# Kernel tuning notes

Hardware: AMD Instinct MI355X
Metric: run time of the kernel (lower is better)

The kernel has to match this reference:

```python
import jax, jax.numpy as jnp
import numpy as np

DIMS = [128, 118, 109, 100, 92]  # dims[i+1] = max(int(dims[i]/1.081), 6)
NUM_SHELLS = 3
TARGET_COORD = 1.081
NUM_BASINS = 8
BATCH = 12288


def _pdist(a, b):
    # Euclidean pairwise distances [Na, Nb]
    a2 = jnp.sum(a * a, axis=-1)
    b2 = jnp.sum(b * b, axis=-1)
    d2 = a2[:, None] + b2[None, :] - 2.0 * (a @ b.T)
    return jnp.sqrt(jnp.clip(d2, 0.0, None))


def setup_inputs() -> dict:
    key = jax.random.key(0)
    ks = jax.random.split(key, 32)
    inp = {"x": jax.random.normal(ks[0], (BATCH, DIMS[0]), jnp.float32)}
    i = 1
    for s in range(4):
        din, dout = DIMS[s], DIMS[s + 1]
        sc = 1.0 / np.sqrt(din)
        inp[f"cw{s}"] = jax.random.uniform(ks[i], (dout, din), jnp.float32, -sc, sc); i += 1
        inp[f"cb{s}"] = jax.random.uniform(ks[i], (dout,), jnp.float32, -sc, sc); i += 1
        sc0 = 1.0 / np.sqrt(DIMS[0])
        inp[f"sw{s}"] = jax.random.uniform(ks[i], (dout, DIMS[0]), jnp.float32, -sc0, sc0); i += 1
        inp[f"sb{s}"] = jax.random.uniform(ks[i], (dout,), jnp.float32, -sc0, sc0); i += 1
    D = DIMS[-1]
    inp["shell_bnd"] = jnp.linspace(0.5, 2.0, NUM_SHELLS + 1, dtype=jnp.float32)
    scs = 1.0 / np.sqrt(NUM_SHELLS)
    inp["se_w"] = jax.random.uniform(ks[i], (D, NUM_SHELLS), jnp.float32, -scs, scs); i += 1
    inp["se_b"] = jax.random.uniform(ks[i], (D,), jnp.float32, -scs, scs); i += 1
    inp["basin_c"] = jax.random.normal(ks[i], (NUM_BASINS, D), jnp.float32) * 0.1; i += 1
    inp["basin_d"] = jnp.linspace(-6.48, -7.68, NUM_BASINS, dtype=jnp.float32)
    inp["basin_w"] = jnp.ones((NUM_BASINS,), jnp.float32) * 0.5
    return inp


def _forward(x, cws, cbs, sws, sbs, shell_bnd, se_w, se_b, basin_c, basin_d, basin_w):
    # CompressionTransform: Linear -> GELU (+ 0.1 * skip from input)
    cur = x
    for w, b, w2, b2 in zip(cws, cbs, sws, sbs):
        cur = jax.nn.gelu(cur @ w.T + b, approximate=False) + 0.1 * (x @ w2.T + b2)
    compressed = cur  # [B, 92]

    # EnergyLandscape: softmax basin mixture
    bdists = _pdist(compressed, basin_c)             # [B, num_basins]
    widths = jax.nn.softplus(basin_w)                # [num_basins]
    basin_probs = jax.nn.softmax(-bdists / widths, axis=-1)
    energy = jnp.sum(basin_probs * basin_d, axis=-1)  # [B]

    # CoordinationAnalysis: pairwise-distance shell histogram
    B = compressed.shape[0]
    dself = _pdist(compressed, compressed)           # [B, B]
    offdiag = ~jnp.eye(B, dtype=bool)
    bnd = jax.nn.softplus(shell_bnd)
    occ = jnp.stack(
        [jnp.sum(jnp.where(offdiag & (dself >= bnd[i]) & (dself < bnd[i + 1]), 1.0, 0.0), axis=-1)
         for i in range(NUM_SHELLS)],
        axis=-1,
    )  # [B, num_shells]
    occ = occ / (TARGET_COORD * (B - 1) + 1e-08)
    feats = compressed + occ @ se_w.T + se_b          # features with coordination info
    return feats, energy, basin_probs, occ


def reference(x, cw0, cb0, sw0, sb0, cw1, cb1, sw1, sb1, cw2, cb2, sw2, sb2,
              cw3, cb3, sw3, sb3, shell_bnd, se_w, se_b, basin_c, basin_d, basin_w):
    cws = [cw0, cw1, cw2, cw3]
    cbs = [cb0, cb1, cb2, cb3]
    sws = [sw0, sw1, sw2, sw3]
    sbs = [sb0, sb1, sb2, sb3]
    return _forward(x, cws, cbs, sws, sbs, shell_bnd, se_w, se_b, basin_c, basin_d, basin_w)
```

## Files before the change

kernel.cpp:

```cpp
#include <hip/hip_runtime.h>
#include <hip/hip_bf16.h>

typedef __attribute__((ext_vector_type(8))) short bf16x8;
typedef __attribute__((ext_vector_type(4))) float f32x4;
typedef unsigned short u16;

#define BATCH 12288

__device__ __forceinline__ u16 f2bf(float f){
  __hip_bfloat16 h = __float2bfloat16(f);
  return *reinterpret_cast<u16*>(&h);
}
__device__ __forceinline__ float bf2f(u16 u){
  __hip_bfloat16 h; *reinterpret_cast<u16*>(&h) = u;
  return __bfloat162float(h);
}
__device__ __forceinline__ f32x4 mfma16(bf16x8 a, bf16x8 b, f32x4 c){
  return __builtin_amdgcn_mfma_f32_16x16x32_bf16(a, b, c, 0, 0, 0);
}
__device__ __forceinline__ float softplusf(float v){ return log1pf(expf(v)); }

__global__ __launch_bounds__(256) void k_wconv8(
    const float* __restrict__ s0, const float* __restrict__ s1,
    const float* __restrict__ s2, const float* __restrict__ s3,
    const float* __restrict__ s4, const float* __restrict__ s5,
    const float* __restrict__ s6, const float* __restrict__ s7,
    u16* __restrict__ dst)
{
  int blk = blockIdx.x;
  int slab = blk >> 6;
  const float* src; int rows, cols;
  switch (slab){
    case 0: src = s0; rows = 118; cols = 128; break;
    case 1: src = s1; rows = 118; cols = 128; break;
    case 2: src = s2; rows = 109; cols = 118; break;
    case 3: src = s3; rows = 109; cols = 128; break;
    case 4: src = s4; rows = 100; cols = 109; break;
    case 5: src = s5; rows = 100; cols = 128; break;
    case 6: src = s6; rows =  92; cols = 100; break;
    default: src = s7; rows =  92; cols = 128; break;
  }
  int idx = (blk & 63) * 256 + threadIdx.x;
  int r = idx >> 7, c = idx & 127;
  float v = (r < rows && c < cols) ? src[r * cols + c] : 0.f;
  dst[slab * 16384 + idx] = f2bf(v);
}

__global__ __launch_bounds__(256) void k_mlp(const float* __restrict__ x,
    const u16* __restrict__ slabs,
    const float* __restrict__ cb0, const float* __restrict__ cb1,
    const float* __restrict__ cb2, const float* __restrict__ cb3,
    const float* __restrict__ sb0, const float* __restrict__ sb1,
    const float* __restrict__ sb2, const float* __restrict__ sb3,
    float* __restrict__ comp)
{
  const int LSTR = 136;
  __shared__ u16 xbf[32 * 136];
  __shared__ u16 act[2][32 * 136];
  int tid = threadIdx.x;
  int lane = tid & 63, w = tid >> 6;
  int fr = lane & 15, fg = lane >> 4;
  int r0 = blockIdx.x * 32;

  #pragma unroll
  for (int i = 0; i < 4; i++){
    int slot = tid + i * 256;
    int row = slot >> 5, c4 = slot & 31;
    float4 v = *reinterpret_cast<const float4*>(&x[(r0 + row) * 128 + c4 * 4]);
    ushort4 pk;
    pk.x = f2bf(v.x); pk.y = f2bf(v.y); pk.z = f2bf(v.z); pk.w = f2bf(v.w);
    *reinterpret_cast<ushort4*>(&xbf[row * LSTR + c4 * 4]) = pk;
  }
  __syncthreads();

  bf16x8 xa[2][4];
  #pragma unroll
  for (int mf = 0; mf < 2; mf++)
    #pragma unroll
    for (int kc = 0; kc < 4; kc++)
      xa[mf][kc] = *reinterpret_cast<const bf16x8*>(&xbf[(16*mf + fr) * LSTR + kc*32 + fg*8]);

  const float* cbs[4] = {cb0, cb1, cb2, cb3};
  const float* sbs[4] = {sb0, sb1, sb2, sb3};
  const int douts[4] = {118, 109, 100, 92};

  #pragma unroll
  for (int s = 0; s < 4; s++){
    const u16* aIn  = (s == 0) ? xbf : &act[(s + 1) & 1][0];
    u16*       aOut = &act[s & 1][0];
    const u16* cwS = slabs + (2*s)     * 16384;
    const u16* swS = slabs + (2*s + 1) * 16384;
    const float* cb = cbs[s];
    const float* sb = sbs[s];
    int dout = douts[s];

    bf16x8 af[2][4];
    #pragma unroll
    for (int mf = 0; mf < 2; mf++)
      #pragma unroll
      for (int kc = 0; kc < 4; kc++)
        af[mf][kc] = *reinterpret_cast<const bf16x8*>(&aIn[(16*mf + fr) * LSTR + kc*32 + fg*8]);

    f32x4 ac1[2][2], ac2[2][2];
    #pragma unroll
    for (int mf = 0; mf < 2; mf++)
      #pragma unroll
      for (int nf = 0; nf < 2; nf++){
        ac1[mf][nf] = (f32x4){0.f,0.f,0.f,0.f};
        ac2[mf][nf] = (f32x4){0.f,0.f,0.f,0.f};
      }

    #pragma unroll
    for (int nf = 0; nf < 2; nf++){
      int o = 32*w + 16*nf + fr;
      #pragma unroll
      for (int kc = 0; kc < 4; kc++){
        bf16x8 b1 = *reinterpret_cast<const bf16x8*>(&cwS[o * 128 + kc*32 + fg*8]);
        bf16x8 b2 = *reinterpret_cast<const bf16x8*>(&swS[o * 128 + kc*32 + fg*8]);
        ac1[0][nf] = mfma16(af[0][kc], b1, ac1[0][nf]);
        ac1[1][nf] = mfma16(af[1][kc], b1, ac1[1][nf]);
        ac2[0][nf] = mfma16(xa[0][kc], b2, ac2[0][nf]);
        ac2[1][nf] = mfma16(xa[1][kc], b2, ac2[1][nf]);
      }
    }

    #pragma unroll
    for (int nf = 0; nf < 2; nf++){
      int col = 32*w + 16*nf + fr;
      float cbv = (col < dout) ? cb[col] : 0.f;
      float sbv = (col < dout) ? sb[col] : 0.f;
      #pragma unroll
      for (int mf = 0; mf < 2; mf++){
        #pragma unroll
        for (int r = 0; r < 4; r++){
          float t1 = ac1[mf][nf][r] + cbv;
          float g = 0.5f * t1 * (1.f + erff(t1 * 0.70710678118654752f));
          float v = g + 0.1f * (ac2[mf][nf][r] + sbv);
          int row = 16*mf + fg*4 + r;
          if (s < 3){
            aOut[row * LSTR + col] = (col < dout) ? f2bf(v) : (u16)0;
          } else {
            if (col < 92) comp[(r0 + row) * 92 + col] = v;
          }
        }
      }
    }
    __syncthreads();
  }
}

__global__ __launch_bounds__(256) void k_rowfin(const float* __restrict__ comp,
    u16* __restrict__ Cbf, float* __restrict__ nrm,
    const float* __restrict__ basin_c, const float* __restrict__ basin_d,
    const float* __restrict__ basin_w,
    float* __restrict__ energy_out, float* __restrict__ probs_out)
{
  int tid = threadIdx.x; int lane = tid & 63; int w = tid >> 6;
  int row = blockIdx.x * 4 + w;

  float c0 = comp[row * 92 + lane];
  int d2i = 64 + lane;
  float c1 = (d2i < 92) ? comp[row * 92 + d2i] : 0.f;

  u16 b0 = f2bf(c0);
  u16 b1 = (d2i < 92) ? f2bf(c1) : (u16)0;
  Cbf[row * 96 + lane] = b0;
  if (lane < 32) Cbf[row * 96 + 64 + lane] = b1;

  float f0 = bf2f(b0), f1 = bf2f(b1);
  float ns = f0*f0 + f1*f1;
  #pragma unroll
  for (int m = 1; m < 64; m <<= 1) ns += __shfl_xor(ns, m);
  if (lane == 0) nrm[row] = ns;

  float bd[8];
  #pragma unroll
  for (int b = 0; b < 8; b++){
    float e0 = c0 - basin_c[b * 92 + lane];
    float p = e0 * e0;
    if (d2i < 92){ float e1 = c1 - basin_c[b * 92 + d2i]; p += e1 * e1; }
    #pragma unroll
    for (int m = 1; m < 64; m <<= 1) p += __shfl_xor(p, m);
    bd[b] = sqrtf(p);
  }
  float z[8]; float mx = -1e30f;
  #pragma unroll
  for (int b = 0; b < 8; b++){
    float wd = softplusf(basin_w[b]);
    z[b] = -bd[b] / wd;
    mx = fmaxf(mx, z[b]);
  }
  float p8[8]; float ssum = 0.f;
  #pragma unroll
  for (int b = 0; b < 8; b++){ p8[b] = expf(z[b] - mx); ssum += p8[b]; }
  float inv = 1.f / ssum; float en = 0.f;
  #pragma unroll
  for (int b = 0; b < 8; b++){ p8[b] *= inv; en += p8[b] * basin_d[b]; }

  if (lane == 0) energy_out[row] = en;
  if (lane < 8){
    float v = (lane & 4) ? ((lane & 2) ? ((lane & 1) ? p8[7] : p8[6])
                                       : ((lane & 1) ? p8[5] : p8[4]))
                         : ((lane & 2) ? ((lane & 1) ? p8[3] : p8[2])
                                       : ((lane & 1) ? p8[1] : p8[0]));
    probs_out[row * 8 + lane] = v;
  }
}

__global__ __launch_bounds__(256, 4) void k_pdist(const u16* __restrict__ Cbf,
    const float* __restrict__ nrm, const float* __restrict__ shell_bnd,
    unsigned* __restrict__ cnt)
{
  __shared__ u16 Bs[2][64 * 104];
  __shared__ float Ns[2][64];
  int tid = threadIdx.x; int lane = tid & 63; int w = tid >> 6;
  int fr = lane & 15, fg = lane >> 4;
  int blk = blockIdx.x;
  int ib = blk % 96, jc = blk / 96;
  int i0 = ib * 128, j0 = jc * 384;

  float q0 = softplusf(shell_bnd[0]); q0 *= q0;
  float q1 = softplusf(shell_bnd[1]); q1 *= q1;
  float q2 = softplusf(shell_bnd[2]); q2 *= q2;
  float q3 = softplusf(shell_bnd[3]); q3 *= q3;

  int wrow0 = i0 + 32 * w;
  bf16x8 A[2][3];
  #pragma unroll
  for (int mf = 0; mf < 2; mf++)
    #pragma unroll
    for (int kc = 0; kc < 3; kc++)
      A[mf][kc] = *reinterpret_cast<const bf16x8*>(&Cbf[(wrow0 + 16*mf + fr) * 96 + kc*32 + fg*8]);

  float na[2][4];
  #pragma unroll
  for (int mf = 0; mf < 2; mf++)
    #pragma unroll
    for (int r = 0; r < 4; r++)
      na[mf][r] = nrm[wrow0 + 16*mf + fg*4 + r];

  unsigned c[2][4][4];
  #pragma unroll
  for (int mf = 0; mf < 2; mf++)
    #pragma unroll
    for (int r = 0; r < 4; r++)
      #pragma unroll
      for (int t = 0; t < 4; t++) c[mf][r][t] = 0u;

  auto stage = [&](int st, int p){
    int jr0 = j0 + st * 64;
    #pragma unroll
    for (int t = 0; t < 3; t++){
      int ch = tid + t * 256;
      int rr = ch / 12, sl = ch - rr * 12;
      *reinterpret_cast<bf16x8*>(&Bs[p][rr * 104 + sl * 8]) =
        *reinterpret_cast<const bf16x8*>(&Cbf[(jr0 + rr) * 96 + sl * 8]);
    }
    if (tid < 64) Ns[p][tid] = nrm[jr0 + tid];
  };

  auto hist = [&](f32x4 h0, f32x4 h1, float nb){
    float d2[2][4];
    #pragma unroll
    for (int r = 0; r < 4; r++){
      d2[0][r] = fmaf(-2.f, h0[r], na[0][r] + nb);
      d2[1][r] = fmaf(-2.f, h1[r], na[1][r] + nb);
    }
    float mn = d2[0][0];
    #pragma unroll
    for (int r = 1; r < 4; r++) mn = fminf(mn, d2[0][r]);
    #pragma unroll
    for (int r = 0; r < 4; r++) mn = fminf(mn, d2[1][r]);
    if (__any(mn < q3)){
      #pragma unroll
      for (int mf = 0; mf < 2; mf++)
        #pragma unroll
        for (int r = 0; r < 4; r++){
          float v = d2[mf][r];
          c[mf][r][0] += (v >= q0);
          c[mf][r][1] += (v >= q1);
          c[mf][r][2] += (v >= q2);
          c[mf][r][3] += (v >= q3);
        }
    }
  };

  stage(0, 0);
  __syncthreads();

  f32x4 gp0, gp1; float nbp = 0.f;
  gp0 = (f32x4){0.f,0.f,0.f,0.f}; gp1 = (f32x4){0.f,0.f,0.f,0.f};

  for (int s = 0; s < 6; s++){
    int p = s & 1;
    if (s < 5) stage(s + 1, p ^ 1);

    #pragma unroll
    for (int nt = 0; nt < 4; nt++){
      bf16x8 B0 = *reinterpret_cast<const bf16x8*>(&Bs[p][(nt*16 + fr) * 104 + 0*32 + fg*8]);
      bf16x8 B1 = *reinterpret_cast<const bf16x8*>(&Bs[p][(nt*16 + fr) * 104 + 1*32 + fg*8]);
      bf16x8 B2 = *reinterpret_cast<const bf16x8*>(&Bs[p][(nt*16 + fr) * 104 + 2*32 + fg*8]);
      float nb = Ns[p][nt*16 + fr];

      f32x4 g0 = (f32x4){0.f,0.f,0.f,0.f};
      f32x4 g1 = (f32x4){0.f,0.f,0.f,0.f};
      g0 = mfma16(A[0][0], B0, g0); g0 = mfma16(A[0][1], B1, g0); g0 = mfma16(A[0][2], B2, g0);
      g1 = mfma16(A[1][0], B0, g1); g1 = mfma16(A[1][1], B1, g1); g1 = mfma16(A[1][2], B2, g1);

      if (nt > 0 || s > 0) hist(gp0, gp1, nbp);

      gp0 = g0; gp1 = g1; nbp = nb;
    }
    __syncthreads();
  }
  hist(gp0, gp1, nbp);

  #pragma unroll
  for (int mf = 0; mf < 2; mf++)
    #pragma unroll
    for (int r = 0; r < 4; r++)
      #pragma unroll
      for (int t = 0; t < 4; t++){
        int v = (int)c[mf][r][t];
        v += __shfl_xor(v, 1); v += __shfl_xor(v, 2);
        v += __shfl_xor(v, 4); v += __shfl_xor(v, 8);
        c[mf][r][t] = (unsigned)v;
      }
  if (fr == 0){
    #pragma unroll
    for (int mf = 0; mf < 2; mf++)
      #pragma unroll
      for (int r = 0; r < 4; r++){
        int row = wrow0 + 16*mf + fg*4 + r;
        #pragma unroll
        for (int s = 0; s < 3; s++){
          unsigned o = c[mf][r][s] - c[mf][r][s + 1];
          if (o) atomicAdd(&cnt[row * 3 + s], o);
        }
      }
  }
}

__global__ __launch_bounds__(256) void k_feats(const float* __restrict__ comp,
    const unsigned* __restrict__ cnt, const float* __restrict__ se_w,
    const float* __restrict__ se_b, float* __restrict__ feats_out,
    float* __restrict__ occ_out)
{
  int tid = threadIdx.x; int lane = tid & 63; int w = tid >> 6;
  int row = blockIdx.x * 4 + w;
  const float denom = 1.081f * 12287.0f + 1e-8f;

  float o0 = (float)cnt[row * 3 + 0] / denom;
  float o1 = (float)cnt[row * 3 + 1] / denom;
  float o2 = (float)cnt[row * 3 + 2] / denom;

  {
    int d = lane;
    float v = comp[row * 92 + d]
            + o0 * se_w[d * 3 + 0] + o1 * se_w[d * 3 + 1] + o2 * se_w[d * 3 + 2]
            + se_b[d];
    feats_out[row * 92 + d] = v;
  }
  int d2 = lane + 64;
  if (d2 < 92){
    float v = comp[row * 92 + d2]
            + o0 * se_w[d2 * 3 + 0] + o1 * se_w[d2 * 3 + 1] + o2 * se_w[d2 * 3 + 2]
            + se_b[d2];
    feats_out[row * 92 + d2] = v;
  }
  if (lane < 3){
    float ov = (lane == 0) ? o0 : ((lane == 1) ? o1 : o2);
    occ_out[row * 3 + lane] = ov;
  }
}

extern "C" void kernel_launch(void* const* d_in, const int* in_sizes, int n_in,
                              void* d_out, int out_size, void* d_ws, size_t ws_size,
                              hipStream_t stream) {
  (void)in_sizes; (void)n_in; (void)out_size; (void)ws_size;

  const float* x = (const float*)d_in[0];
  const float* cw[4] = {(const float*)d_in[1], (const float*)d_in[5], (const float*)d_in[9],  (const float*)d_in[13]};
  const float* cb[4] = {(const float*)d_in[2], (const float*)d_in[6], (const float*)d_in[10], (const float*)d_in[14]};
  const float* sw[4] = {(const float*)d_in[3], (const float*)d_in[7], (const float*)d_in[11], (const float*)d_in[15]};
  const float* sb[4] = {(const float*)d_in[4], (const float*)d_in[8], (const float*)d_in[12], (const float*)d_in[16]};
  const float* shell_bnd = (const float*)d_in[17];
  const float* se_w = (const float*)d_in[18];
  const float* se_b = (const float*)d_in[19];
  const float* basin_c = (const float*)d_in[20];
  const float* basin_d = (const float*)d_in[21];
  const float* basin_w = (const float*)d_in[22];

  char* ws = (char*)d_ws;
  float*    comp  = (float*)(ws);
  u16*      Cbf   = (u16*)  (ws + 4521984);
  float*    nrm   = (float*)(ws + 6881280);
  unsigned* cnt   = (unsigned*)(ws + 6930432);
  u16*      slabs = (u16*)  (ws + 7077888);

  float* out = (float*)d_out;
  float* feats_out  = out;
  float* energy_out = out + 1130496;
  float* probs_out  = out + 1142784;
  float* occ_out    = out + 1241088;

  hipMemsetAsync(cnt, 0, 147456, stream);

  k_wconv8<<<512, 256, 0, stream>>>(cw[0], sw[0], cw[1], sw[1], cw[2], sw[2], cw[3], sw[3],
                                    slabs);

  k_mlp<<<384, 256, 0, stream>>>(x, slabs,
      cb[0], cb[1], cb[2], cb[3], sb[0], sb[1], sb[2], sb[3], comp);

  k_rowfin<<<3072, 256, 0, stream>>>(comp, Cbf, nrm, basin_c, basin_d, basin_w,
                                     energy_out, probs_out);

  k_pdist<<<3072, 256, 0, stream>>>(Cbf, nrm, shell_bnd, cnt);

  k_feats<<<3072, 256, 0, stream>>>(comp, cnt, se_w, se_b, feats_out, occ_out);
}
```

Baseline: 143.8 us.

## Fold norms into MFMA accumulator and register-stage pdist tile loads

Row norms are stored as -0.5*|x|^2 so the pairwise-distance test becomes a comparison of (hr + hc + dot) against -0.5*q^2. The norm sum is used as the MFMA initial accumulator, which removes the per-element fma. The global-to-LDS staging is split into a register load issued before the compute and an LDS write after it, so the global load latency overlaps the MFMAs. The __any early-out and the one-tile software pipeline of the histogram are dropped, and comparisons are now done unconditionally. This removes a branch at the cost of always doing the compares, and the negated scaling could shift rounding at the shell boundaries.

```diff
diff --git a/kernel.cpp b/kernel.cpp
--- a/kernel.cpp
+++ b/kernel.cpp
@@ -150,7 +150,7 @@
 }
 
 __global__ __launch_bounds__(256) void k_rowfin(const float* __restrict__ comp,
-    u16* __restrict__ Cbf, float* __restrict__ nrm,
+    u16* __restrict__ Cbf, float* __restrict__ nrm2,
     const float* __restrict__ basin_c, const float* __restrict__ basin_d,
     const float* __restrict__ basin_w,
     float* __restrict__ energy_out, float* __restrict__ probs_out)
@@ -171,7 +171,7 @@
   float ns = f0*f0 + f1*f1;
   #pragma unroll
   for (int m = 1; m < 64; m <<= 1) ns += __shfl_xor(ns, m);
-  if (lane == 0) nrm[row] = ns;
+  if (lane == 0) nrm2[row] = -0.5f * ns;
 
   float bd[8];
   #pragma unroll
@@ -208,7 +208,7 @@
 }
 
 __global__ __launch_bounds__(256, 4) void k_pdist(const u16* __restrict__ Cbf,
-    const float* __restrict__ nrm, const float* __restrict__ shell_bnd,
+    const float* __restrict__ nrm2, const float* __restrict__ shell_bnd,
     unsigned* __restrict__ cnt)
 {
   __shared__ u16 Bs[2][64 * 104];
@@ -219,10 +219,10 @@
   int ib = blk % 96, jc = blk / 96;
   int i0 = ib * 128, j0 = jc * 384;
 
-  float q0 = softplusf(shell_bnd[0]); q0 *= q0;
-  float q1 = softplusf(shell_bnd[1]); q1 *= q1;
-  float q2 = softplusf(shell_bnd[2]); q2 *= q2;
-  float q3 = softplusf(shell_bnd[3]); q3 *= q3;
+  float q0 = softplusf(shell_bnd[0]); float mq0 = -0.5f * q0 * q0;
+  float q1 = softplusf(shell_bnd[1]); float mq1 = -0.5f * q1 * q1;
+  float q2 = softplusf(shell_bnd[2]); float mq2 = -0.5f * q2 * q2;
+  float q3 = softplusf(shell_bnd[3]); float mq3 = -0.5f * q3 * q3;
 
   int wrow0 = i0 + 32 * w;
   bf16x8 A[2][3];
@@ -232,12 +232,12 @@
     for (int kc = 0; kc < 3; kc++)
       A[mf][kc] = *reinterpret_cast<const bf16x8*>(&Cbf[(wrow0 + 16*mf + fr) * 96 + kc*32 + fg*8]);
 
-  float na[2][4];
+  float hr[2][4];
   #pragma unroll
   for (int mf = 0; mf < 2; mf++)
     #pragma unroll
     for (int r = 0; r < 4; r++)
-      na[mf][r] = nrm[wrow0 + 16*mf + fg*4 + r];
+      hr[mf][r] = nrm2[wrow0 + 16*mf + fg*4 + r];
 
   unsigned c[2][4][4];
   #pragma unroll
@@ -247,73 +247,69 @@
       #pragma unroll
       for (int t = 0; t < 4; t++) c[mf][r][t] = 0u;
 
-  auto stage = [&](int st, int p){
+  int ofsL[3], ofsR[3], ofsS[3];
+  #pragma unroll
+  for (int t = 0; t < 3; t++){
+    int ch = tid + t * 256;
+    int rr = ch / 12, sl = ch - rr * 12;
+    ofsR[t] = rr; ofsS[t] = sl * 8;
+    ofsL[t] = rr * 104 + sl * 8;
+  }
+
+  bf16x8 rv[3]; float nsv = 0.f;
+  auto stage_load = [&](int st){
     int jr0 = j0 + st * 64;
     #pragma unroll
-    for (int t = 0; t < 3; t++){
-      int ch = tid + t * 256;
-      int rr = ch / 12, sl = ch - rr * 12;
-      *reinterpret_cast<bf16x8*>(&Bs[p][rr * 104 + sl * 8]) =
-        *reinterpret_cast<const bf16x8*>(&Cbf[(jr0 + rr) * 96 + sl * 8]);
-    }
-    if (tid < 64) Ns[p][tid] = nrm[jr0 + tid];
+    for (int t = 0; t < 3; t++)
+      rv[t] = *reinterpret_cast<const bf16x8*>(&Cbf[(jr0 + ofsR[t]) * 96 + ofsS[t]]);
+    if (tid < 64) nsv = nrm2[jr0 + tid];
   };
-
-  auto hist = [&](f32x4 h0, f32x4 h1, float nb){
-    float d2[2][4];
-    #pragma unroll
-    for (int r = 0; r < 4; r++){
-      d2[0][r] = fmaf(-2.f, h0[r], na[0][r] + nb);
-      d2[1][r] = fmaf(-2.f, h1[r], na[1][r] + nb);
-    }
-    float mn = d2[0][0];
-    #pragma unroll
-    for (int r = 1; r < 4; r++) mn = fminf(mn, d2[0][r]);
-    #pragma unroll
-    for (int r = 0; r < 4; r++) mn = fminf(mn, d2[1][r]);
-    if (__any(mn < q3)){
-      #pragma unroll
-      for (int mf = 0; mf < 2; mf++)
-        #pragma unroll
-        for (int r = 0; r < 4; r++){
-          float v = d2[mf][r];
-          c[mf][r][0] += (v >= q0);
-          c[mf][r][1] += (v >= q1);
-          c[mf][r][2] += (v >= q2);
-          c[mf][r][3] += (v >= q3);
-        }
-    }
+  auto stage_write = [&](int p){
+    #pragma unroll
+    for (int t = 0; t < 3; t++)
+      *reinterpret_cast<bf16x8*>(&Bs[p][ofsL[t]]) = rv[t];
+    if (tid < 64) Ns[p][tid] = nsv;
   };
 
-  stage(0, 0);
+  stage_load(0); stage_write(0);
   __syncthreads();
-
-  f32x4 gp0, gp1; float nbp = 0.f;
-  gp0 = (f32x4){0.f,0.f,0.f,0.f}; gp1 = (f32x4){0.f,0.f,0.f,0.f};
 
   for (int s = 0; s < 6; s++){
     int p = s & 1;
-    if (s < 5) stage(s + 1, p ^ 1);
+    if (s < 5) stage_load(s + 1);
 
     #pragma unroll
     for (int nt = 0; nt < 4; nt++){
       bf16x8 B0 = *reinterpret_cast<const bf16x8*>(&Bs[p][(nt*16 + fr) * 104 + 0*32 + fg*8]);
       bf16x8 B1 = *reinterpret_cast<const bf16x8*>(&Bs[p][(nt*16 + fr) * 104 + 1*32 + fg*8]);
       bf16x8 B2 = *reinterpret_cast<const bf16x8*>(&Bs[p][(nt*16 + fr) * 104 + 2*32 + fg*8]);
-      float nb = Ns[p][nt*16 + fr];
-
-      f32x4 g0 = (f32x4){0.f,0.f,0.f,0.f};
-      f32x4 g1 = (f32x4){0.f,0.f,0.f,0.f};
+      float hc = Ns[p][nt*16 + fr];
+
+      f32x4 g0, g1;
+      #pragma unroll
+      for (int r = 0; r < 4; r++){ g0[r] = hr[0][r] + hc; g1[r] = hr[1][r] + hc; }
       g0 = mfma16(A[0][0], B0, g0); g0 = mfma16(A[0][1], B1, g0); g0 = mfma16(A[0][2], B2, g0);
       g1 = mfma16(A[1][0], B0, g1); g1 = mfma16(A[1][1], B1, g1); g1 = mfma16(A[1][2], B2, g1);
 
-      if (nt > 0 || s > 0) hist(gp0, gp1, nbp);
-
-      gp0 = g0; gp1 = g1; nbp = nb;
+      #pragma unroll
+      for (int r = 0; r < 4; r++){
+        float v0 = g0[r], v1 = g1[r];
+        c[0][r][0] += (v0 <= mq0);
+        c[0][r][1] += (v0 <= mq1);
+        c[0][r][2] += (v0 <= mq2);
+        c[0][r][3] += (v0 <= mq3);
+        c[1][r][0] += (v1 <= mq0);
+        c[1][r][1] += (v1 <= mq1);
+        c[1][r][2] += (v1 <= mq2);
+        c[1][r][3] += (v1 <= mq3);
+      }
     }
-    __syncthreads();
-  }
-  hist(gp0, gp1, nbp);
+
+    if (s < 5){
+      stage_write(p ^ 1);
+      __syncthreads();
+    }
+  }
 
   #pragma unroll
   for (int mf = 0; mf < 2; mf++)
@@ -394,7 +390,7 @@
   char* ws = (char*)d_ws;
   float*    comp  = (float*)(ws);
   u16*      Cbf   = (u16*)  (ws + 4521984);
-  float*    nrm   = (float*)(ws + 6881280);
+  float*    nrm2  = (float*)(ws + 6881280);
   unsigned* cnt   = (unsigned*)(ws + 6930432);
   u16*      slabs = (u16*)  (ws + 7077888);
 
@@ -412,10 +408,10 @@
   k_mlp<<<384, 256, 0, stream>>>(x, slabs,
       cb[0], cb[1], cb[2], cb[3], sb[0], sb[1], sb[2], sb[3], comp);
 
-  k_rowfin<<<3072, 256, 0, stream>>>(comp, Cbf, nrm, basin_c, basin_d, basin_w,
+  k_rowfin<<<3072, 256, 0, stream>>>(comp, Cbf, nrm2, basin_c, basin_d, basin_w,
                                      energy_out, probs_out);
 
-  k_pdist<<<3072, 256, 0, stream>>>(Cbf, nrm, shell_bnd, cnt);
+  k_pdist<<<3072, 256, 0, stream>>>(Cbf, nrm2, shell_bnd, cnt);
 
   k_feats<<<3072, 256, 0, stream>>>(comp, cnt, se_w, se_b, feats_out, occ_out);
 }
```

Measured after the change: 211.7 us. 1.47x slower.
